# Optimization experiments

Hardware: AMD Instinct MI355X
Metric: run time of the kernel (lower is better)

Reference implementation:

```python
import jax, jax.numpy as jnp
import numpy as np

N_HEADS = 16
D_MODEL = 1024
SEQ = 1024
WIDTH = 32
BATCH = 4


def _make_graph(n, w, seed=0):
    # Mirrors sparse_attention_graph: normal offsets around each node index,
    # mod n, then per-row duplicates are replaced by global-ish tokens 0,1,...
    rng = np.random.default_rng(seed)
    pulls = rng.normal(0.0, float(w), size=(n, w)).astype(np.int64)
    adj = (pulls + np.arange(n)[:, None]) % n
    rows = []
    for r in adj:
        u = np.unique(r)
        i = 0
        while u.shape[0] < w:
            d = w - u.shape[0]
            u = np.unique(np.concatenate([np.arange(i, i + d), u]))
            i += d
        rows.append(np.sort(u))
    return jnp.asarray(np.stack(rows), dtype=jnp.int32)


def setup_inputs() -> dict:
    key = jax.random.key(0)
    ks = jax.random.split(key, 5)
    scale = 1.0 / np.sqrt(D_MODEL).astype(np.float32)
    return {
        "hidden_states": jax.random.normal(ks[0], (BATCH, SEQ, D_MODEL), jnp.float32),
        "wq_kernel": jax.random.normal(ks[1], (D_MODEL, D_MODEL), jnp.float32) * scale,
        "wq_bias": jnp.zeros((D_MODEL,), jnp.float32),
        "wk_kernel": jax.random.normal(ks[2], (D_MODEL, D_MODEL), jnp.float32) * scale,
        "wk_bias": jnp.zeros((D_MODEL,), jnp.float32),
        "wv_kernel": jax.random.normal(ks[3], (D_MODEL, D_MODEL), jnp.float32) * scale,
        "wv_bias": jnp.zeros((D_MODEL,), jnp.float32),
        "wo_kernel": jax.random.normal(ks[4], (D_MODEL, D_MODEL), jnp.float32) * scale,
        "wo_bias": jnp.zeros((D_MODEL,), jnp.float32),
        "graph": _make_graph(SEQ, WIDTH),
    }


def reference(hidden_states, wq_kernel, wq_bias, wk_kernel, wk_bias,
              wv_kernel, wv_bias, wo_kernel, wo_bias, graph):
    B, N, D = hidden_states.shape
    H = N_HEADS
    depth = D // H

    def split_heads(x):
        return x.reshape(B, N, H, depth).transpose(0, 2, 1, 3)  # [B,H,N,depth]

    q = split_heads(hidden_states @ wq_kernel + wq_bias)
    k = split_heads(hidden_states @ wk_kernel + wk_bias)
    v = split_heads(hidden_states @ wv_kernel + wv_bias)

    # Gather neighbor keys per node: [B,H,N,W,depth]; dot only on graph edges.
    kg = k[:, :, graph, :]
    dots = jnp.einsum('bhnd,bhnwd->bhnw', q, kg)

    # Scatter edge dots into dense [B,H,N,N] score matrix; non-edges stay 0,
    # exactly as dot_circle_product does (softmax then runs over the FULL row).
    rows = jnp.arange(N)[:, None]  # broadcasts with graph [N,W]
    scores = jnp.zeros((B, H, N, N), hidden_states.dtype).at[:, :, rows, graph].set(dots)

    attn = jax.nn.softmax(scores / jnp.sqrt(jnp.asarray(depth, scores.dtype)), axis=-1)
    out = jnp.einsum('bhij,bhjd->bhid', attn, v)          # [B,H,N,depth]
    out = out.transpose(0, 2, 1, 3).reshape(B, N, D)      # merge heads
    output = out @ wo_kernel + wo_bias
    return (output, attn)
```

## Files before the change

### kernel.cpp

```cpp
#include <hip/hip_runtime.h>
#include <hip/hip_bf16.h>

constexpr int B = 4;
constexpr int N = 1024;
constexpr int D = 1024;
constexpr int H = 16;
constexpr int DEPTH = 64;
constexpr int W = 32;
constexpr int LDQKV = 3072;
constexpr int SROWS = 12288;

typedef _Float16 f16x8 __attribute__((ext_vector_type(8)));
typedef float f32x4 __attribute__((ext_vector_type(4)));
typedef unsigned short us8 __attribute__((ext_vector_type(8)));
typedef unsigned short us4 __attribute__((ext_vector_type(4)));

__device__ __forceinline__ float h2f(unsigned short u) {
  return (float)__builtin_bit_cast(_Float16, u);
}

__device__ __forceinline__ void load_lds16(const void* g, void* l) {
  unsigned int lo = (unsigned int)(unsigned long long)l;
  __builtin_amdgcn_global_load_lds(
      (const __attribute__((address_space(1))) unsigned int*)g,
      (__attribute__((address_space(3))) unsigned int*)lo, 16, 0, 0);
}

__global__ __launch_bounds__(256) void prep_all(
    const float* __restrict__ hidden, const float* __restrict__ wq,
    const float* __restrict__ wk, const float* __restrict__ wv,
    const float* __restrict__ wo, const float* __restrict__ bq,
    const float* __restrict__ bk, const float* __restrict__ bv,
    unsigned short* __restrict__ A16, unsigned short* __restrict__ BTh,
    unsigned short* __restrict__ WoTh, float* __restrict__ biasq) {
  __shared__ float sf[64][65];
  const int t = threadIdx.x;
  int blk = blockIdx.x;

  if (blk < 2048) {
    const size_t i = ((size_t)blk * 256 + t) * 8;
    float4 a = *(const float4*)(hidden + i);
    float4 b = *(const float4*)(hidden + i + 4);
    float xs[8] = {a.x, a.y, a.z, a.w, b.x, b.y, b.z, b.w};
    us8 hv;
#pragma unroll
    for (int j = 0; j < 8; j++)
      hv[j] = __builtin_bit_cast(unsigned short, (_Float16)xs[j]);
    *(us8*)(A16 + i) = hv;
    return;
  }
  blk -= 2048;
  if (blk < 1024) {
    const int which = blk >> 8;
    const int sub = blk & 255;
    const float* w = which == 0 ? wq : which == 1 ? wk : which == 2 ? wv : wo;
    unsigned short* oh = which < 3 ? BTh : WoTh;
    const int rowOff = which < 3 ? which * 1024 : 0;

    const int tn = (sub & 15) * 64;
    const int tk = (sub >> 4) * 64;
#pragma unroll
    for (int i = 0; i < 4; i++) {
      int f = i * 256 + t;
      int r = f >> 4, c4 = (f & 15) * 4;
      float4 v = *(const float4*)(w + (size_t)(tk + r) * 1024 + tn + c4);
      sf[r][c4 + 0] = v.x; sf[r][c4 + 1] = v.y;
      sf[r][c4 + 2] = v.z; sf[r][c4 + 3] = v.w;
    }
    __syncthreads();
    const int n = t >> 2;
    const int kc = (t & 3) * 16;
    us8 hv[2];
#pragma unroll
    for (int half = 0; half < 2; half++) {
#pragma unroll
      for (int j = 0; j < 8; j++) {
        float x = sf[kc + half * 8 + j][n];
        hv[half][j] = __builtin_bit_cast(unsigned short, (_Float16)x);
      }
    }
    size_t dst = (size_t)(rowOff + tn + n) * 1024 + tk + kc;
    *(us8*)(oh + dst) = hv[0];
    *(us8*)(oh + dst + 8) = hv[1];
    return;
  }
  blk -= 1024;
  int i = blk * 256 + t;
  biasq[i] = i < 1024 ? bq[i] : (i < 2048 ? bk[i - 1024] : bv[i - 2048]);
}

__global__ __launch_bounds__(256, 2) void gemm_qkv(
    const unsigned short* __restrict__ A16, const unsigned short* __restrict__ BTh,
    const float* __restrict__ bias, unsigned short* __restrict__ Cout,
    int K, int Nn) {
  __shared__ __align__(16) unsigned short sA[2 * 128 * 32];
  __shared__ __align__(16) unsigned short sB[2 * 256 * 32];

  const int tid = threadIdx.x;
  const int lane = tid & 63;
  const int wave = tid >> 6;
  const int wr = wave >> 1, wc = wave & 1;

  const int gx = gridDim.x;
  const int nwg = gx * gridDim.y;
  int bid = blockIdx.y * gx + blockIdx.x;
  bid = (bid & 7) * (nwg >> 3) + (bid >> 3);
  const int bm = (bid / gx) * 128;
  const int bn = (bid % gx) * 256;

  size_t aoff[2];
  int ldsA[2];
#pragma unroll
  for (int c = 0; c < 2; c++) {
    const int chunk = wave + 4 * c;
    const int e = chunk * 512 + lane * 8;
    const int r = e >> 5;
    const int kpos = (e >> 3) & 3;
    const int ksrc = kpos ^ ((r >> 1) & 3);
    aoff[c] = (size_t)(bm + r) * K + ksrc * 8;
    ldsA[c] = chunk * 512;
  }
  size_t boff[4];
  int ldsB[4];
#pragma unroll
  for (int c = 0; c < 4; c++) {
    const int chunk = wave + 4 * c;
    const int e = chunk * 512 + lane * 8;
    const int r = e >> 5;
    const int kpos = (e >> 3) & 3;
    const int ksrc = kpos ^ ((r >> 1) & 3);
    boff[c] = (size_t)(bn + r) * K + ksrc * 8;
    ldsB[c] = chunk * 512;
  }

  const int fr = lane & 15;
  const int fkg = lane >> 4;

  int aroff[4], broff[8];
#pragma unroll
  for (int m = 0; m < 4; m++) {
    const int ra = wr * 64 + m * 16 + fr;
    aroff[m] = ra * 32 + ((fkg ^ ((ra >> 1) & 3)) << 3);
  }
#pragma unroll
  for (int n = 0; n < 8; n++) {
    const int rb = wc * 128 + n * 16 + fr;
    broff[n] = rb * 32 + ((fkg ^ ((rb >> 1) & 3)) << 3);
  }

  f32x4 acc[4][8] = {};

  const int NT = K >> 5;
#pragma unroll
  for (int c = 0; c < 2; c++) load_lds16(A16 + aoff[c], sA + ldsA[c]);
#pragma unroll
  for (int c = 0; c < 4; c++) load_lds16(BTh + boff[c], sB + ldsB[c]);
  __syncthreads();

  int cur = 0;
  for (int t = 0; t < NT; t++) {
    const int boA = cur * (128 * 32);
    const int boB = cur * (256 * 32);
    const int nxA = (cur ^ 1) * (128 * 32);
    const int nxB = (cur ^ 1) * (256 * 32);
    if (t + 1 < NT) {
      const int k0 = (t + 1) << 5;
#pragma unroll
      for (int c = 0; c < 2; c++) load_lds16(A16 + aoff[c] + k0, sA + nxA + ldsA[c]);
#pragma unroll
      for (int c = 0; c < 4; c++) load_lds16(BTh + boff[c] + k0, sB + nxB + ldsB[c]);
    }
    f16x8 a[4], bh[8];
#pragma unroll
    for (int m = 0; m < 4; m++) a[m] = *(const f16x8*)(sA + boA + aroff[m]);
#pragma unroll
    for (int n = 0; n < 8; n++) bh[n] = *(const f16x8*)(sB + boB + broff[n]);
    __builtin_amdgcn_s_setprio(1);
#pragma unroll
    for (int m = 0; m < 4; m++)
#pragma unroll
      for (int n = 0; n < 8; n++)
        acc[m][n] = __builtin_amdgcn_mfma_f32_16x16x32_f16(a[m], bh[n], acc[m][n], 0, 0, 0);
    __builtin_amdgcn_s_setprio(0);
    __syncthreads();
    cur ^= 1;
  }

#pragma unroll
  for (int m = 0; m < 4; m++) {
    const int row = bm + wr * 64 + m * 16 + fkg * 4;
#pragma unroll
    for (int n = 0; n < 8; n++) {
      const int col = bn + wc * 128 + n * 16 + fr;
      const float bsv = bias[col];
#pragma unroll
      for (int j = 0; j < 4; j++) {
        const float v = acc[m][n][j] + bsv;
        Cout[(size_t)(row + j) * Nn + col] =
            __builtin_bit_cast(unsigned short, (_Float16)v);
      }
    }
  }
}

__global__ __launch_bounds__(256, 4) void gemm_o(
    const unsigned short* __restrict__ A16, const unsigned short* __restrict__ BTh,
    const float* __restrict__ bias, float* __restrict__ Cout, int K, int Nn) {
  __shared__ __align__(16) unsigned short sA[2 * 128 * 32];
  __shared__ __align__(16) unsigned short sB[2 * 128 * 32];

  const int tid = threadIdx.x;
  const int lane = tid & 63;
  const int wave = tid >> 6;
  const int wr = wave >> 1, wc = wave & 1;

  const int gx = gridDim.x;
  const int nwg = gx * gridDim.y;
  int bid = blockIdx.y * gx + blockIdx.x;
  bid = (bid & 7) * (nwg >> 3) + (bid >> 3);
  const int bm = (bid / gx) * 128;
  const int bn = (bid % gx) * 128;

  size_t aoff[2], boff[2];
  int ldsoff[2];
#pragma unroll
  for (int c = 0; c < 2; c++) {
    const int chunk = wave + 4 * c;
    const int e = chunk * 512 + lane * 8;
    const int r = e >> 5;
    const int kpos = (e >> 3) & 3;
    const int ksrc = kpos ^ ((r >> 1) & 3);
    aoff[c] = (size_t)(bm + r) * K + ksrc * 8;
    boff[c] = (size_t)(bn + r) * K + ksrc * 8;
    ldsoff[c] = chunk * 512;
  }

  const int fr = lane & 15;
  const int fkg = lane >> 4;

  int aroff[4], broff[4];
#pragma unroll
  for (int m = 0; m < 4; m++) {
    const int ra = wr * 64 + m * 16 + fr;
    aroff[m] = ra * 32 + ((fkg ^ ((ra >> 1) & 3)) << 3);
    const int rb = wc * 64 + m * 16 + fr;
    broff[m] = rb * 32 + ((fkg ^ ((rb >> 1) & 3)) << 3);
  }

  f32x4 acc[4][4] = {};

  const int NT = K >> 5;
#pragma unroll
  for (int c = 0; c < 2; c++) {
    load_lds16(A16 + aoff[c], sA + ldsoff[c]);
    load_lds16(BTh + boff[c], sB + ldsoff[c]);
  }
  __syncthreads();

  int cur = 0;
  for (int t = 0; t < NT; t++) {
    const int bo_ = cur * (128 * 32);
    const int nx_ = (cur ^ 1) * (128 * 32);
    if (t + 1 < NT) {
      const int k0 = (t + 1) << 5;
#pragma unroll
      for (int c = 0; c < 2; c++) {
        load_lds16(A16 + aoff[c] + k0, sA + nx_ + ldsoff[c]);
        load_lds16(BTh + boff[c] + k0, sB + nx_ + ldsoff[c]);
      }
    }
    f16x8 a[4], bh[4];
#pragma unroll
    for (int m = 0; m < 4; m++) a[m] = *(const f16x8*)(sA + bo_ + aroff[m]);
#pragma unroll
    for (int n = 0; n < 4; n++) bh[n] = *(const f16x8*)(sB + bo_ + broff[n]);
    __builtin_amdgcn_s_setprio(1);
#pragma unroll
    for (int m = 0; m < 4; m++)
#pragma unroll
      for (int n = 0; n < 4; n++)
        acc[m][n] = __builtin_amdgcn_mfma_f32_16x16x32_f16(a[m], bh[n], acc[m][n], 0, 0, 0);
    __builtin_amdgcn_s_setprio(0);
    __syncthreads();
    cur ^= 1;
  }

#pragma unroll
  for (int m = 0; m < 4; m++) {
    const int row = bm + wr * 64 + m * 16 + fkg * 4;
#pragma unroll
    for (int n = 0; n < 4; n++) {
      const int col = bn + wc * 64 + n * 16 + fr;
      const float bsv = bias[col];
#pragma unroll
      for (int j = 0; j < 4; j++)
        Cout[(size_t)(row + j) * Nn + col] = acc[m][n][j] + bsv;
    }
  }
}

__global__ __launch_bounds__(256) void vsum_part(const unsigned short* __restrict__ v,
                                                 float* __restrict__ part) {
  const int b = blockIdx.x >> 4;
  const int chunk = blockIdx.x & 15;
  const int d4 = threadIdx.x * 4;
  const unsigned short* p =
      v + (size_t)b * N * LDQKV + (size_t)chunk * 64 * LDQKV + d4;
  float4 s = {0.f, 0.f, 0.f, 0.f};
#pragma unroll 8
  for (int n = 0; n < 64; n++) {
    us4 t = *(const us4*)(p + (size_t)n * LDQKV);
    s.x += h2f(t[0]); s.y += h2f(t[1]); s.z += h2f(t[2]); s.w += h2f(t[3]);
  }
  *(float4*)(part + (size_t)blockIdx.x * 1024 + d4) = s;
}

__global__ __launch_bounds__(256) void vsum_comb(const float* __restrict__ part,
                                                 float* __restrict__ vsum) {
  const int i = blockIdx.x * 256 + threadIdx.x;
  const int b = i >> 10, d = i & 1023;
  float s = 0.f;
#pragma unroll
  for (int c = 0; c < 16; c++) s += part[(size_t)(b * 16 + c) * 1024 + d];
  vsum[i] = s;
}

__global__ __launch_bounds__(256) void attn_pass1(
    const unsigned short* __restrict__ qkv16, const float* __restrict__ vsum,
    const int* __restrict__ graph, float* __restrict__ pbuf,
    float* __restrict__ basebuf, unsigned short* __restrict__ O16,
    float* __restrict__ attn) {
  const int blk = blockIdx.x;
  const int n = blk & (N - 1);
  const int hg = (blk >> 10) & 3;
  const int b = blk >> 12;
  const int wave = threadIdx.x >> 6;
  const int lane = threadIdx.x & 63;
  const int h = hg * 4 + wave;
  const int bid = (b * H + h) * N + n;

  __shared__ float q_sh[4][DEPTH];
  __shared__ int g_sh[W];
  __shared__ float p_sh[4][W];
  __shared__ float rowbuf[4][N];

  const unsigned short* qrow = qkv16 + (size_t)(b * N + n) * LDQKV + h * DEPTH;
  q_sh[wave][lane] = h2f(qrow[lane]);
  if (threadIdx.x < W) g_sh[threadIdx.x] = graph[n * W + threadIdx.x];
  __syncthreads();

  const int w = lane >> 1;
  const int half = lane & 1;
  const unsigned short* krow =
      qkv16 + 1024 + (size_t)(b * N + g_sh[w]) * LDQKV + h * DEPTH + half * 32;
  float acc = 0.f;
#pragma unroll
  for (int j8 = 0; j8 < 4; j8++) {
    us8 kv = *(const us8*)(krow + j8 * 8);
    const float* qh = &q_sh[wave][half * 32 + j8 * 8];
#pragma unroll
    for (int e = 0; e < 8; e++) acc += h2f(kv[e]) * qh[e];
  }
  acc += __shfl_xor(acc, 1);
  const float dot = acc * 0.125f;

  float m = dot;
#pragma unroll
  for (int off = 2; off < 64; off <<= 1) m = fmaxf(m, __shfl_xor(m, off));
  m = fmaxf(m, 0.f);

  const float e = expf(dot - m);
  float s = e;
#pragma unroll
  for (int off = 1; off < 64; off <<= 1) s += __shfl_xor(s, off);
  s *= 0.5f;

  const float em = expf(-m);
  const float Z = (float)(N - W) * em + s;
  const float inv = 1.f / Z;
  const float base = em * inv;
  const float pw = e * inv;

  if (half == 0) p_sh[wave][w] = pw;
  __syncthreads();

  const bool fused = (bid >= SROWS);
  if (!fused) {
    if (half == 0) pbuf[(size_t)bid * W + w] = pw;
    if (lane == 0) basebuf[bid] = base;
  }

  const unsigned short* vbase = qkv16 + 2048;
  const int col = h * DEPTH + lane;
  float ov = base * vsum[b * D + col];
#pragma unroll 4
  for (int ww = 0; ww < W; ww++) {
    ov += (p_sh[wave][ww] - base) *
          h2f(vbase[(size_t)(b * N + g_sh[ww]) * LDQKV + col]);
  }
  _Float16 hh = (_Float16)ov;
  O16[(size_t)(b * N + n) * D + col] = __builtin_bit_cast(unsigned short, hh);

  if (fused) {
    f32x4* rw = (f32x4*)rowbuf[wave];
    f32x4 b4v = {base, base, base, base};
#pragma unroll
    for (int i = 0; i < 4; i++) rw[lane + 64 * i] = b4v;
    __syncthreads();
    if (half == 0) rowbuf[wave][g_sh[w]] = pw;
    __syncthreads();
    f32x4* dst = (f32x4*)(attn + (size_t)bid * N);
#pragma unroll
    for (int i = 0; i < 4; i++)
      __builtin_nontemporal_store(rw[lane + 64 * i], dst + lane + 64 * i);
  }
}

__global__ __launch_bounds__(256) void attn_fill_rem(
    const float* __restrict__ pbuf, const float* __restrict__ basebuf,
    const int* __restrict__ graph, float* __restrict__ attn) {
  const int blk = blockIdx.x;
  const int n = blk & (N - 1);
  const int hh = blk >> 10;
  const int t = threadIdx.x;

  __shared__ float row[2][N];
  __shared__ int g_sh[W];

  const int bid0 = hh * N + n;
  const int bid1 = (hh + 6) * N + n;

  if (t < W) g_sh[t] = graph[n * W + t];
  const float base0 = basebuf[bid0];
  const float base1 = basebuf[bid1];
  f32x4* row40 = (f32x4*)row[0];
  f32x4* row41 = (f32x4*)row[1];
  row40[t] = (f32x4){base0, base0, base0, base0};
  row41[t] = (f32x4){base1, base1, base1, base1};
  __syncthreads();
  if (t < 2 * W) {
    const int r = t >> 5;
    const int w = t & 31;
    const int bidr = r == 0 ? bid0 : bid1;
    row[r][g_sh[w]] = pbuf[(size_t)bidr * W + w];
  }
  __syncthreads();
  __builtin_nontemporal_store(row40[t], (f32x4*)(attn + (size_t)bid0 * N) + t);
  __builtin_nontemporal_store(row41[t], (f32x4*)(attn + (size_t)bid1 * N) + t);
}

extern "C" void kernel_launch(void* const* d_in, const int* in_sizes, int n_in,
                              void* d_out, int out_size, void* d_ws, size_t ws_size,
                              hipStream_t stream) {
  const float* hidden = (const float*)d_in[0];
  const float* wq = (const float*)d_in[1];
  const float* bq = (const float*)d_in[2];
  const float* wk = (const float*)d_in[3];
  const float* bk = (const float*)d_in[4];
  const float* wv = (const float*)d_in[5];
  const float* bv = (const float*)d_in[6];
  const float* wo = (const float*)d_in[7];
  const float* bo = (const float*)d_in[8];
  const int* graph = (const int*)d_in[9];

  float* out0 = (float*)d_out;
  float* attnp = out0 + (size_t)B * N * D;

  const size_t M1 = (size_t)1024 * 1024;
  unsigned short* qkv16 = (unsigned short*)attnp;
  unsigned short* A16 = (unsigned short*)(attnp + 6 * M1);
  unsigned short* BTh = (unsigned short*)(attnp + 8 * M1);
  unsigned short* WoTh = (unsigned short*)(attnp + 9 * M1 + 524288);
  unsigned short* O16 = (unsigned short*)(attnp + 10 * M1);

  float* pbuf = (float*)d_ws;
  float* basebuf = pbuf + (size_t)B * H * N * W;
  float* vsumb = basebuf + (size_t)B * H * N;
  float* biasq = pbuf;
  float* vpart = pbuf + 4096;

  prep_all<<<3084, 256, 0, stream>>>(hidden, wq, wk, wv, wo, bq, bk, bv,
                                     A16, BTh, WoTh, biasq);

  gemm_qkv<<<dim3(12, 32), 256, 0, stream>>>(A16, BTh, biasq, qkv16,
                                             1024, 3072);

  vsum_part<<<64, 256, 0, stream>>>(qkv16 + 2048, vpart);
  vsum_comb<<<16, 256, 0, stream>>>(vpart, vsumb);

  attn_pass1<<<B * 4 * N, 256, 0, stream>>>(qkv16, vsumb, graph, pbuf, basebuf,
                                            O16, attnp);

  gemm_o<<<dim3(8, 32), 256, 0, stream>>>(O16, WoTh, bo, out0, 1024, 1024);

  attn_fill_rem<<<SROWS / 2, 256, 0, stream>>>(pbuf, basebuf, graph, attnp);
}
```

Measured before the change: 154.4 us.

## Fuse V column-sum into QKV GEMM epilogue and rebalance attention row split

The V column sums are now reduced inside the QKV GEMM epilogue from the fp32 accumulators, and the bias contribution is added in vsum_comb, so the separate vsum_part kernel and its re-read of V disappear. SROWS drops from 12288 to 10240, so attn_pass1 writes more dense attention rows directly and attn_fill_rem handles fewer. The O16 buffer is aliased onto A16 to save memory. The row-buffer fill and its barriers in attn_pass1 now run in every block, not only fused ones, which adds some sync cost to non-fused blocks. The GEMM epilogue also gains an extra barrier and shuffles.

```diff
diff --git a/kernel.cpp b/kernel.cpp
--- a/kernel.cpp
+++ b/kernel.cpp
@@ -8,7 +8,7 @@
 constexpr int DEPTH = 64;
 constexpr int W = 32;
 constexpr int LDQKV = 3072;
-constexpr int SROWS = 12288;
+constexpr int SROWS = 10240;
 
 typedef _Float16 f16x8 __attribute__((ext_vector_type(8)));
 typedef float f32x4 __attribute__((ext_vector_type(4)));
@@ -92,9 +92,10 @@
 __global__ __launch_bounds__(256, 2) void gemm_qkv(
     const unsigned short* __restrict__ A16, const unsigned short* __restrict__ BTh,
     const float* __restrict__ bias, unsigned short* __restrict__ Cout,
-    int K, int Nn) {
+    float* __restrict__ vpart, int K, int Nn) {
   __shared__ __align__(16) unsigned short sA[2 * 128 * 32];
   __shared__ __align__(16) unsigned short sB[2 * 256 * 32];
+  __shared__ float vred[2][2][8][16];
 
   const int tid = threadIdx.x;
   const int lane = tid & 63;
@@ -198,6 +199,33 @@
         const float v = acc[m][n][j] + bsv;
         Cout[(size_t)(row + j) * Nn + col] =
             __builtin_bit_cast(unsigned short, (_Float16)v);
+      }
+    }
+  }
+
+  if (bn >= 2048) {
+    float csum[8];
+#pragma unroll
+    for (int n = 0; n < 8; n++) {
+      float s = 0.f;
+#pragma unroll
+      for (int m = 0; m < 4; m++)
+#pragma unroll
+        for (int j = 0; j < 4; j++) s += acc[m][n][j];
+      s += __shfl_xor(s, 16);
+      s += __shfl_xor(s, 32);
+      csum[n] = s;
+    }
+    if (fkg == 0) {
+#pragma unroll
+      for (int n = 0; n < 8; n++) vred[wr][wc][n][fr] = csum[n];
+    }
+    __syncthreads();
+    if (wr == 0 && fkg == 0) {
+#pragma unroll
+      for (int n = 0; n < 8; n++) {
+        const int d = bn - 2048 + wc * 128 + n * 16 + fr;
+        vpart[(size_t)(bm >> 7) * 1024 + d] = csum[n] + vred[1][wc][n][fr];
       }
     }
   }
@@ -299,29 +327,14 @@
   }
 }
 
-__global__ __launch_bounds__(256) void vsum_part(const unsigned short* __restrict__ v,
-                                                 float* __restrict__ part) {
-  const int b = blockIdx.x >> 4;
-  const int chunk = blockIdx.x & 15;
-  const int d4 = threadIdx.x * 4;
-  const unsigned short* p =
-      v + (size_t)b * N * LDQKV + (size_t)chunk * 64 * LDQKV + d4;
-  float4 s = {0.f, 0.f, 0.f, 0.f};
-#pragma unroll 8
-  for (int n = 0; n < 64; n++) {
-    us4 t = *(const us4*)(p + (size_t)n * LDQKV);
-    s.x += h2f(t[0]); s.y += h2f(t[1]); s.z += h2f(t[2]); s.w += h2f(t[3]);
-  }
-  *(float4*)(part + (size_t)blockIdx.x * 1024 + d4) = s;
-}
-
-__global__ __launch_bounds__(256) void vsum_comb(const float* __restrict__ part,
+__global__ __launch_bounds__(256) void vsum_comb(const float* __restrict__ vpart,
+                                                 const float* __restrict__ biasq,
                                                  float* __restrict__ vsum) {
   const int i = blockIdx.x * 256 + threadIdx.x;
   const int b = i >> 10, d = i & 1023;
-  float s = 0.f;
-#pragma unroll
-  for (int c = 0; c < 16; c++) s += part[(size_t)(b * 16 + c) * 1024 + d];
+  float s = 1024.0f * biasq[2048 + d];
+#pragma unroll
+  for (int c = 0; c < 8; c++) s += vpart[(size_t)(b * 8 + c) * 1024 + d];
   vsum[i] = s;
 }
 
@@ -401,14 +414,14 @@
   _Float16 hh = (_Float16)ov;
   O16[(size_t)(b * N + n) * D + col] = __builtin_bit_cast(unsigned short, hh);
 
+  f32x4* rw = (f32x4*)rowbuf[wave];
+  f32x4 b4v = {base, base, base, base};
+#pragma unroll
+  for (int i = 0; i < 4; i++) rw[lane + 64 * i] = b4v;
+  __syncthreads();
+  if (fused && half == 0) rowbuf[wave][g_sh[w]] = pw;
+  __syncthreads();
   if (fused) {
-    f32x4* rw = (f32x4*)rowbuf[wave];
-    f32x4 b4v = {base, base, base, base};
-#pragma unroll
-    for (int i = 0; i < 4; i++) rw[lane + 64 * i] = b4v;
-    __syncthreads();
-    if (half == 0) rowbuf[wave][g_sh[w]] = pw;
-    __syncthreads();
     f32x4* dst = (f32x4*)(attn + (size_t)bid * N);
 #pragma unroll
     for (int i = 0; i < 4; i++)
@@ -428,7 +441,7 @@
   __shared__ int g_sh[W];
 
   const int bid0 = hh * N + n;
-  const int bid1 = (hh + 6) * N + n;
+  const int bid1 = (hh + 5) * N + n;
 
   if (t < W) g_sh[t] = graph[n * W + t];
   const float base0 = basebuf[bid0];
@@ -469,9 +482,9 @@
   const size_t M1 = (size_t)1024 * 1024;
   unsigned short* qkv16 = (unsigned short*)attnp;
   unsigned short* A16 = (unsigned short*)(attnp + 6 * M1);
+  unsigned short* O16 = A16;
   unsigned short* BTh = (unsigned short*)(attnp + 8 * M1);
   unsigned short* WoTh = (unsigned short*)(attnp + 9 * M1 + 524288);
-  unsigned short* O16 = (unsigned short*)(attnp + 10 * M1);
 
   float* pbuf = (float*)d_ws;
   float* basebuf = pbuf + (size_t)B * H * N * W;
@@ -482,11 +495,10 @@
   prep_all<<<3084, 256, 0, stream>>>(hidden, wq, wk, wv, wo, bq, bk, bv,
                                      A16, BTh, WoTh, biasq);
 
-  gemm_qkv<<<dim3(12, 32), 256, 0, stream>>>(A16, BTh, biasq, qkv16,
+  gemm_qkv<<<dim3(12, 32), 256, 0, stream>>>(A16, BTh, biasq, qkv16, vpart,
                                              1024, 3072);
 
-  vsum_part<<<64, 256, 0, stream>>>(qkv16 + 2048, vpart);
-  vsum_comb<<<16, 256, 0, stream>>>(vpart, vsumb);
+  vsum_comb<<<16, 256, 0, stream>>>(vpart, biasq, vsumb);
 
   attn_pass1<<<B * 4 * N, 256, 0, stream>>>(qkv16, vsumb, graph, pbuf, basebuf,
                                             O16, attnp);
```

Result: faster. 148.8 us (-3.6%).
